# Kernel optimization log

Hardware: AMD Instinct MI355X
Metric: run time of the kernel (lower is better)

Reference implementation:

```python
import jax, jax.numpy as jnp
import numpy as np

B, N, DIN, DOUT, L = 32, 512, 768, 256, 512
NEG = -9.0e15
SLOPE = 0.2  # LeakyReLU negative slope


def setup_inputs() -> dict:
    key = jax.random.key(0)
    ks = jax.random.split(key, 7)
    h = jax.random.normal(ks[0], (B, N, DIN), dtype=jnp.float32)
    adj = jax.random.randint(ks[1], (B, N, N), 0, 2, dtype=jnp.int32)
    positions = jax.random.randint(ks[2], (B, N), 0, L, dtype=jnp.int32)
    W = jax.random.normal(ks[3], (DIN, DOUT), dtype=jnp.float32) * 0.02
    a1 = jax.random.normal(ks[4], (DOUT,), dtype=jnp.float32) * 0.02
    a2 = jax.random.normal(ks[5], (DOUT,), dtype=jnp.float32) * 0.02
    pos_table = jax.random.normal(ks[6], (L, DOUT), dtype=jnp.float32) * 0.02
    return {"h": h, "adj": adj, "positions": positions, "W": W,
            "a1": a1, "a2": a2, "pos_table": pos_table}


def reference(h, adj, positions, W, a1, a2, pos_table):
    # Wh = W(h) + pos_emb(positions)   -> [B, N, DOUT]
    Wh = jnp.einsum('bnd,de->bne', h, W) + pos_table[positions]
    # Pairwise GAT score: e_ij = leakyrelu(a1 . Wh_i + a2 . Wh_j)
    # (identical math to concat([Wh_i, Wh_j]) @ [a1; a2], without the O(N^2*2D) tensor)
    s1 = jnp.einsum('bnd,d->bn', Wh, a1)  # source term   [B, N]
    s2 = jnp.einsum('bnd,d->bn', Wh, a2)  # target term   [B, N]
    e = jax.nn.leaky_relu(s1[:, :, None] + s2[:, None, :], negative_slope=SLOPE)  # [B,N,N]
    # adjacency mask + softmax over neighbors (dropout is identity in eval)
    attention = jax.nn.softmax(jnp.where(adj > 0, e, NEG), axis=-1)  # [B, N, N]
    h_prime = jnp.einsum('bij,bjd->bid', attention, Wh)  # [B, N, DOUT]
    return h_prime, attention
```

## Files before the change

kernel.cpp:

```cpp
#include <hip/hip_runtime.h>
#include <math.h>

#define B 32
#define N 512
#define DIN 768
#define DOUT 256
#define NEGV -9.0e15f
#define SLOPE 0.2f

typedef __bf16 bf16x8 __attribute__((ext_vector_type(8)));
typedef float f32x4 __attribute__((ext_vector_type(4)));
typedef unsigned short us8 __attribute__((ext_vector_type(8)));

__device__ __forceinline__ unsigned short f2b(float f) {
    union { float f; unsigned u; } v; v.f = f;
    unsigned r = v.u + 0x7FFF + ((v.u >> 16) & 1);
    return (unsigned short)(r >> 16);
}

__device__ __forceinline__ void gload_lds16(const unsigned short* g, unsigned short* l) {
    __builtin_amdgcn_global_load_lds(
        (const __attribute__((address_space(1))) unsigned int*)(unsigned long long)(uintptr_t)g,
        (__attribute__((address_space(3))) unsigned int*)(uintptr_t)l,
        16, 0, 0);
}

__global__ __launch_bounds__(256) void conv_fused(
    const float4* __restrict__ hin, ushort4* __restrict__ hout,
    const float* __restrict__ W, unsigned short* __restrict__ WT) {
    __shared__ unsigned short tile[64][65];
    const int t = threadIdx.x;
    if (blockIdx.x < 12288) {
        int idx = blockIdx.x * 256 + t;
        float4 v = hin[idx];
        ushort4 o;
        o.x = f2b(v.x); o.y = f2b(v.y); o.z = f2b(v.z); o.w = f2b(v.w);
        hout[idx] = o;
    } else {
        int bid = blockIdx.x - 12288;
        int k0 = (bid % 12) * 64, n0 = (bid / 12) * 64;
        const int cl = t & 63, cg = t >> 6;
#pragma unroll
        for (int i = 0; i < 16; ++i) {
            int k = cg * 16 + i;
            tile[cl][k] = f2b(W[(size_t)(k0 + k) * DOUT + n0 + cl]);
        }
        __syncthreads();
#pragma unroll
        for (int i = 0; i < 16; ++i) {
            int n = cg * 16 + i;
            WT[(size_t)(n0 + n) * DIN + k0 + cl] = tile[n][cl];
        }
    }
}

__global__ __launch_bounds__(256) void wh_mfma(
    const unsigned short* __restrict__ hA,
    const unsigned short* __restrict__ WT,
    const int*   __restrict__ pos,
    const float* __restrict__ ptab,
    const float* __restrict__ a1,
    const float* __restrict__ a2,
    unsigned short* __restrict__ WhT,
    float* __restrict__ s1, float* __restrict__ s2)
{
    constexpr int K = DIN;
    __shared__ unsigned short smem[12288];
    unsigned short* As = smem;
    unsigned short* Bs = smem + 8192;
    unsigned short* tileT = smem;

    const int t    = threadIdx.x;
    const int lane = t & 63;
    const int w    = t >> 6;
    const int lin  = blockIdx.x;
    const int m0   = (lin & 127) * 128;
    const int n0   = (lin >> 7) * 64;

    int arow[4], apos[4];
#pragma unroll
    for (int i = 0; i < 4; ++i) {
        int c = i * 256 + t;
        arow[i] = c >> 3;
        apos[i] = (c & 7) ^ ((c >> 3) & 7);
    }
    int brow[2], bpos[2];
#pragma unroll
    for (int i = 0; i < 2; ++i) {
        int c = i * 256 + t;
        brow[i] = c >> 3;
        bpos[i] = (c & 7) ^ ((c >> 3) & 7);
    }
    const unsigned short* gA[4];
    const unsigned short* gB[2];
#pragma unroll
    for (int i = 0; i < 4; ++i) gA[i] = hA + (size_t)(m0 + arow[i]) * K + apos[i] * 8;
#pragma unroll
    for (int i = 0; i < 2; ++i) gB[i] = WT + (size_t)(n0 + brow[i]) * K + bpos[i] * 8;
    unsigned short* lA[4];
    unsigned short* lB[2];
#pragma unroll
    for (int i = 0; i < 4; ++i) lA[i] = As + (i * 256 + (t & 192)) * 8;
#pragma unroll
    for (int i = 0; i < 2; ++i) lB[i] = Bs + (i * 256 + (t & 192)) * 8;

    const int wm = (w & 1) * 64, wn = (w >> 1) * 32;
    const int l15 = lane & 15, q = lane >> 4;
    int aoff[2][4], boff[2][2];
#pragma unroll
    for (int kk = 0; kk < 2; ++kk) {
        int pg = kk * 4 + q;
#pragma unroll
        for (int i = 0; i < 4; ++i) {
            int rm = wm + i * 16 + l15;
            aoff[kk][i] = rm * 64 + ((pg ^ (rm & 7)) * 8);
        }
#pragma unroll
        for (int i = 0; i < 2; ++i) {
            int rn = wn + i * 16 + l15;
            boff[kk][i] = rn * 64 + ((pg ^ (rn & 7)) * 8);
        }
    }

    f32x4 acc[4][2];
#pragma unroll
    for (int i = 0; i < 4; ++i)
#pragma unroll
        for (int j = 0; j < 2; ++j) acc[i][j] = (f32x4){0.f, 0.f, 0.f, 0.f};

    for (int k0 = 0; k0 < K; k0 += 64) {
#pragma unroll
        for (int i = 0; i < 4; ++i) gload_lds16(gA[i] + k0, lA[i]);
#pragma unroll
        for (int i = 0; i < 2; ++i) gload_lds16(gB[i] + k0, lB[i]);
        __syncthreads();
#pragma unroll
        for (int kk = 0; kk < 2; ++kk) {
            bf16x8 af[4], bfr[2];
#pragma unroll
            for (int i = 0; i < 4; ++i) af[i] = *(const bf16x8*)(As + aoff[kk][i]);
#pragma unroll
            for (int i = 0; i < 2; ++i) bfr[i] = *(const bf16x8*)(Bs + boff[kk][i]);
#pragma unroll
            for (int mi = 0; mi < 4; ++mi)
#pragma unroll
                for (int ni = 0; ni < 2; ++ni)
                    acc[mi][ni] = __builtin_amdgcn_mfma_f32_16x16x32_bf16(
                        af[mi], bfr[ni], acc[mi][ni], 0, 0, 0);
        }
        __syncthreads();
    }

    const float a1v[2] = { a1[n0 + wn + l15], a1[n0 + wn + 16 + l15] };
    const float a2v[2] = { a2[n0 + wn + l15], a2[n0 + wn + 16 + l15] };
#pragma unroll
    for (int mi = 0; mi < 4; ++mi) {
        const int jb = wm + mi * 16 + q * 4;
        float v[2][4];
#pragma unroll
        for (int ni = 0; ni < 2; ++ni) {
            const int nl = wn + ni * 16 + l15;
            ushort4 pk;
            unsigned short* pp = (unsigned short*)&pk;
#pragma unroll
            for (int r = 0; r < 4; ++r) {
                int m = m0 + jb + r;
                int p = pos[m];
                float val = acc[mi][ni][r] + ptab[(size_t)p * DOUT + n0 + nl];
                v[ni][r] = val;
                pp[r] = f2b(val);
            }
            *(ushort4*)&tileT[nl * 136 + jb] = pk;
        }
#pragma unroll
        for (int r = 0; r < 4; ++r) {
            float t1 = v[0][r] * a1v[0] + v[1][r] * a1v[1];
            float t2 = v[0][r] * a2v[0] + v[1][r] * a2v[1];
#pragma unroll
            for (int mk = 1; mk < 16; mk <<= 1) {
                t1 += __shfl_xor(t1, mk);
                t2 += __shfl_xor(t2, mk);
            }
            if (l15 == 0) {
                atomicAdd(&s1[m0 + jb + r], t1);
                atomicAdd(&s2[m0 + jb + r], t2);
            }
        }
    }
    __syncthreads();
    const int bb = m0 >> 9, j0 = m0 & 511;
#pragma unroll
    for (int rr = 0; rr < 4; ++rr) {
        int nl = (t >> 4) + rr * 16;
        int jl = (t & 15) * 8;
        us8 vv = *(const us8*)&tileT[nl * 136 + jl];
        *(us8*)&WhT[((size_t)bb * DOUT + n0 + nl) * N + j0 + jl] = vv;
    }
}

__global__ __launch_bounds__(1024) void attn_hp(
    const float* __restrict__ s1,
    const float* __restrict__ s2,
    const int*   __restrict__ adj,
    const unsigned short* __restrict__ WhT,
    float* __restrict__ att,
    float* __restrict__ hp)
{
    __shared__ unsigned short P[64 * 512];

    const int t    = threadIdx.x;
    const int lane = t & 63;
    const int w    = t >> 6;
    const int xid  = blockIdx.x & 7;
    const int rid  = blockIdx.x >> 3;
    const int bb   = xid * 4 + (rid >> 3);
    const int m0   = (rid & 7) * 64;

    {
        const int r = t >> 4, c = t & 15;
        const size_t rowg = (size_t)bb * N + m0 + r;
        const float s1i = s1[rowg];
        const int4*   adjp = (const int4*)(adj + rowg * N) + c;
        const float4* s2p  = (const float4*)(s2 + (size_t)bb * N) + c;

        unsigned msk = 0u;
        float mx = -3.0e38f;
#pragma unroll
        for (int i = 0; i < 8; ++i) {
            int4 a = adjp[i * 16];
            float4 sv = s2p[i * 16];
            float v0 = s1i + sv.x; v0 = v0 > 0.f ? v0 : SLOPE * v0;
            float v1 = s1i + sv.y; v1 = v1 > 0.f ? v1 : SLOPE * v1;
            float v2 = s1i + sv.z; v2 = v2 > 0.f ? v2 : SLOPE * v2;
            float v3 = s1i + sv.w; v3 = v3 > 0.f ? v3 : SLOPE * v3;
            v0 = (a.x > 0) ? v0 : NEGV;
            v1 = (a.y > 0) ? v1 : NEGV;
            v2 = (a.z > 0) ? v2 : NEGV;
            v3 = (a.w > 0) ? v3 : NEGV;
            unsigned bits = (a.x > 0 ? 1u : 0u) | (a.y > 0 ? 2u : 0u) |
                            (a.z > 0 ? 4u : 0u) | (a.w > 0 ? 8u : 0u);
            msk |= bits << (i * 4);
            mx = fmaxf(mx, fmaxf(fmaxf(v0, v1), fmaxf(v2, v3)));
        }
#pragma unroll
        for (int mk = 1; mk < 16; mk <<= 1) mx = fmaxf(mx, __shfl_xor(mx, mk));

        float sum = 0.f;
#pragma unroll
        for (int i = 0; i < 8; ++i) {
            float4 sv = s2p[i * 16];
            float v0 = s1i + sv.x; v0 = v0 > 0.f ? v0 : SLOPE * v0;
            float v1 = s1i + sv.y; v1 = v1 > 0.f ? v1 : SLOPE * v1;
            float v2 = s1i + sv.z; v2 = v2 > 0.f ? v2 : SLOPE * v2;
            float v3 = s1i + sv.w; v3 = v3 > 0.f ? v3 : SLOPE * v3;
            v0 = ((msk >> (i * 4 + 0)) & 1) ? v0 : NEGV;
            v1 = ((msk >> (i * 4 + 1)) & 1) ? v1 : NEGV;
            v2 = ((msk >> (i * 4 + 2)) & 1) ? v2 : NEGV;
            v3 = ((msk >> (i * 4 + 3)) & 1) ? v3 : NEGV;
            sum += __expf(v0 - mx) + __expf(v1 - mx) +
                   __expf(v2 - mx) + __expf(v3 - mx);
        }
#pragma unroll
        for (int mk = 1; mk < 16; mk <<= 1) sum += __shfl_xor(sum, mk);
        const float inv = 1.0f / sum;

        float4* attrow = (float4*)(att + rowg * N);
        unsigned short* Prow = P + r * 512;
        const int r7 = r & 7, chalf = (c & 1) * 4;
#pragma unroll
        for (int i = 0; i < 8; ++i) {
            float4 sv = s2p[i * 16];
            float v0 = s1i + sv.x; v0 = v0 > 0.f ? v0 : SLOPE * v0;
            float v1 = s1i + sv.y; v1 = v1 > 0.f ? v1 : SLOPE * v1;
            float v2 = s1i + sv.z; v2 = v2 > 0.f ? v2 : SLOPE * v2;
            float v3 = s1i + sv.w; v3 = v3 > 0.f ? v3 : SLOPE * v3;
            v0 = ((msk >> (i * 4 + 0)) & 1) ? v0 : NEGV;
            v1 = ((msk >> (i * 4 + 1)) & 1) ? v1 : NEGV;
            v2 = ((msk >> (i * 4 + 2)) & 1) ? v2 : NEGV;
            v3 = ((msk >> (i * 4 + 3)) & 1) ? v3 : NEGV;
            float e0 = __expf(v0 - mx) * inv;
            float e1 = __expf(v1 - mx) * inv;
            float e2 = __expf(v2 - mx) * inv;
            float e3 = __expf(v3 - mx) * inv;
            attrow[i * 16 + c] = (float4){e0, e1, e2, e3};
            int slot = i * 8 + (c >> 1);
            int S = slot ^ r7 ^ (slot >> 3);
            ushort4 pk = { f2b(e0), f2b(e1), f2b(e2), f2b(e3) };
            *(ushort4*)&Prow[S * 8 + chalf] = pk;
        }
    }
    __syncthreads();

    const int wn  = w * 16;
    const int l15 = lane & 15, q = lane >> 4;
    const unsigned short* bRow = WhT + ((size_t)bb * DOUT + wn + l15) * N + q * 8;
    int rm7[4], rmBase[4];
#pragma unroll
    for (int mi = 0; mi < 4; ++mi) {
        int rm = mi * 16 + l15;
        rm7[mi] = rm & 7;
        rmBase[mi] = rm * 512;
    }

    f32x4 acc[4];
#pragma unroll
    for (int i = 0; i < 4; ++i) acc[i] = (f32x4){0.f, 0.f, 0.f, 0.f};

#pragma unroll 4
    for (int k0 = 0; k0 < N; k0 += 32) {
        const int slot = (k0 >> 3) + q;
        const int hi = slot >> 3;
        bf16x8 af[4];
        bf16x8 bfr = *(const bf16x8*)(bRow + k0);
#pragma unroll
        for (int mi = 0; mi < 4; ++mi) {
            int S = slot ^ rm7[mi] ^ hi;
            af[mi] = *(const bf16x8*)&P[rmBase[mi] + S * 8];
        }
#pragma unroll
        for (int mi = 0; mi < 4; ++mi)
            acc[mi] = __builtin_amdgcn_mfma_f32_16x16x32_bf16(
                af[mi], bfr, acc[mi], 0, 0, 0);
    }

#pragma unroll
    for (int mi = 0; mi < 4; ++mi) {
#pragma unroll
        for (int rr = 0; rr < 4; ++rr) {
            int m = m0 + mi * 16 + q * 4 + rr;
            int n = wn + l15;
            hp[((size_t)bb * N + m) * DOUT + n] = acc[mi][rr];
        }
    }
}

extern "C" void kernel_launch(void* const* d_in, const int* in_sizes, int n_in,
                              void* d_out, int out_size, void* d_ws, size_t ws_size,
                              hipStream_t stream) {
    const float* h         = (const float*)d_in[0];
    const int*   adj       = (const int*)  d_in[1];
    const int*   positions = (const int*)  d_in[2];
    const float* W         = (const float*)d_in[3];
    const float* a1        = (const float*)d_in[4];
    const float* a2        = (const float*)d_in[5];
    const float* pos_table = (const float*)d_in[6];

    float* out     = (float*)d_out;
    float* h_prime = out;
    float* att     = out + (size_t)B * N * DOUT;

    char* ws = (char*)d_ws;
    unsigned short* h_bf = (unsigned short*)ws;
    unsigned short* WT   = (unsigned short*)(ws + 25165824);
    unsigned short* WhT  = (unsigned short*)(ws + 25559040);
    float*          s1   = (float*)(ws + 33947648);
    float*          s2   = s1 + (size_t)B * N;

    hipMemsetAsync(s1, 0, (size_t)2 * B * N * sizeof(float), stream);
    conv_fused<<<12288 + 48, 256, 0, stream>>>((const float4*)h, (ushort4*)h_bf, W, WT);
    wh_mfma<<<512, 256, 0, stream>>>(h_bf, WT, positions, pos_table, a1, a2, WhT, s1, s2);
    attn_hp<<<256, 1024, 0, stream>>>(s1, s2, adj, WhT, att, h_prime);
}
```

Measured before the change: 164.1 us.

## Fuse fp32-to-bf16 conversion of h into the Wh GEMM A-tile load

Removes the separate pass that converted h to bf16 in a workspace buffer. The GEMM now reads fp32 h directly with register loads, converts to bf16 in registers, and writes the swizzled tile to LDS. This avoids writing and re-reading a 25 MB intermediate. The cost is that the A loads go through registers instead of the async global-to-LDS path, and they read twice the bytes per tile.

```diff
diff --git a/kernel.cpp b/kernel.cpp
--- a/kernel.cpp
+++ b/kernel.cpp
@@ -25,37 +25,28 @@
         16, 0, 0);
 }
 
-__global__ __launch_bounds__(256) void conv_fused(
-    const float4* __restrict__ hin, ushort4* __restrict__ hout,
+__global__ __launch_bounds__(256) void wt_kernel(
     const float* __restrict__ W, unsigned short* __restrict__ WT) {
     __shared__ unsigned short tile[64][65];
     const int t = threadIdx.x;
-    if (blockIdx.x < 12288) {
-        int idx = blockIdx.x * 256 + t;
-        float4 v = hin[idx];
-        ushort4 o;
-        o.x = f2b(v.x); o.y = f2b(v.y); o.z = f2b(v.z); o.w = f2b(v.w);
-        hout[idx] = o;
-    } else {
-        int bid = blockIdx.x - 12288;
-        int k0 = (bid % 12) * 64, n0 = (bid / 12) * 64;
-        const int cl = t & 63, cg = t >> 6;
-#pragma unroll
-        for (int i = 0; i < 16; ++i) {
-            int k = cg * 16 + i;
-            tile[cl][k] = f2b(W[(size_t)(k0 + k) * DOUT + n0 + cl]);
-        }
-        __syncthreads();
-#pragma unroll
-        for (int i = 0; i < 16; ++i) {
-            int n = cg * 16 + i;
-            WT[(size_t)(n0 + n) * DIN + k0 + cl] = tile[n][cl];
-        }
+    int bid = blockIdx.x;
+    int k0 = (bid % 12) * 64, n0 = (bid / 12) * 64;
+    const int cl = t & 63, cg = t >> 6;
+#pragma unroll
+    for (int i = 0; i < 16; ++i) {
+        int k = cg * 16 + i;
+        tile[cl][k] = f2b(W[(size_t)(k0 + k) * DOUT + n0 + cl]);
+    }
+    __syncthreads();
+#pragma unroll
+    for (int i = 0; i < 16; ++i) {
+        int n = cg * 16 + i;
+        WT[(size_t)(n0 + n) * DIN + k0 + cl] = tile[n][cl];
     }
 }
 
 __global__ __launch_bounds__(256) void wh_mfma(
-    const unsigned short* __restrict__ hA,
+    const float* __restrict__ hF,
     const unsigned short* __restrict__ WT,
     const int*   __restrict__ pos,
     const float* __restrict__ ptab,
@@ -77,32 +68,26 @@
     const int m0   = (lin & 127) * 128;
     const int n0   = (lin >> 7) * 64;
 
-    int arow[4], apos[4];
+    const float* gA[4];
+    int aw[4];
 #pragma unroll
     for (int i = 0; i < 4; ++i) {
         int c = i * 256 + t;
-        arow[i] = c >> 3;
-        apos[i] = (c & 7) ^ ((c >> 3) & 7);
-    }
-    int brow[2], bpos[2];
+        int arow = c >> 3;
+        int apos = (c & 7) ^ (arow & 7);
+        gA[i] = hF + (size_t)(m0 + arow) * K + apos * 8;
+        aw[i] = c * 8;
+    }
+    const unsigned short* gB[2];
+    unsigned short* lB[2];
 #pragma unroll
     for (int i = 0; i < 2; ++i) {
         int c = i * 256 + t;
-        brow[i] = c >> 3;
-        bpos[i] = (c & 7) ^ ((c >> 3) & 7);
-    }
-    const unsigned short* gA[4];
-    const unsigned short* gB[2];
-#pragma unroll
-    for (int i = 0; i < 4; ++i) gA[i] = hA + (size_t)(m0 + arow[i]) * K + apos[i] * 8;
-#pragma unroll
-    for (int i = 0; i < 2; ++i) gB[i] = WT + (size_t)(n0 + brow[i]) * K + bpos[i] * 8;
-    unsigned short* lA[4];
-    unsigned short* lB[2];
-#pragma unroll
-    for (int i = 0; i < 4; ++i) lA[i] = As + (i * 256 + (t & 192)) * 8;
-#pragma unroll
-    for (int i = 0; i < 2; ++i) lB[i] = Bs + (i * 256 + (t & 192)) * 8;
+        int brow = c >> 3;
+        int bpos = (c & 7) ^ (brow & 7);
+        gB[i] = WT + (size_t)(n0 + brow) * K + bpos * 8;
+        lB[i] = Bs + (i * 256 + (t & 192)) * 8;
+    }
 
     const int wm = (w & 1) * 64, wn = (w >> 1) * 32;
     const int l15 = lane & 15, q = lane >> 4;
@@ -129,10 +114,23 @@
         for (int j = 0; j < 2; ++j) acc[i][j] = (f32x4){0.f, 0.f, 0.f, 0.f};
 
     for (int k0 = 0; k0 < K; k0 += 64) {
-#pragma unroll
-        for (int i = 0; i < 4; ++i) gload_lds16(gA[i] + k0, lA[i]);
+        float4 f0[4], f1[4];
+#pragma unroll
+        for (int i = 0; i < 4; ++i) {
+            f0[i] = *(const float4*)(gA[i] + k0);
+            f1[i] = *(const float4*)(gA[i] + k0 + 4);
+        }
 #pragma unroll
         for (int i = 0; i < 2; ++i) gload_lds16(gB[i] + k0, lB[i]);
+#pragma unroll
+        for (int i = 0; i < 4; ++i) {
+            union { us8 v; __bf16 b[8]; } p;
+            p.b[0] = (__bf16)f0[i].x; p.b[1] = (__bf16)f0[i].y;
+            p.b[2] = (__bf16)f0[i].z; p.b[3] = (__bf16)f0[i].w;
+            p.b[4] = (__bf16)f1[i].x; p.b[5] = (__bf16)f1[i].y;
+            p.b[6] = (__bf16)f1[i].z; p.b[7] = (__bf16)f1[i].w;
+            *(us8*)(As + aw[i]) = p.v;
+        }
         __syncthreads();
 #pragma unroll
         for (int kk = 0; kk < 2; ++kk) {
@@ -350,14 +348,13 @@
     float* att     = out + (size_t)B * N * DOUT;
 
     char* ws = (char*)d_ws;
-    unsigned short* h_bf = (unsigned short*)ws;
-    unsigned short* WT   = (unsigned short*)(ws + 25165824);
-    unsigned short* WhT  = (unsigned short*)(ws + 25559040);
-    float*          s1   = (float*)(ws + 33947648);
-    float*          s2   = s1 + (size_t)B * N;
+    unsigned short* WT  = (unsigned short*)ws;
+    unsigned short* WhT = (unsigned short*)(ws + 393216);
+    float*          s1  = (float*)(ws + 8781824);
+    float*          s2  = s1 + (size_t)B * N;
 
     hipMemsetAsync(s1, 0, (size_t)2 * B * N * sizeof(float), stream);
-    conv_fused<<<12288 + 48, 256, 0, stream>>>((const float4*)h, (ushort4*)h_bf, W, WT);
-    wh_mfma<<<512, 256, 0, stream>>>(h_bf, WT, positions, pos_table, a1, a2, WhT, s1, s2);
+    wt_kernel<<<48, 256, 0, stream>>>(W, WT);
+    wh_mfma<<<512, 256, 0, stream>>>(h, WT, positions, pos_table, a1, a2, WhT, s1, s2);
     attn_hp<<<256, 1024, 0, stream>>>(s1, s2, adj, WhT, att, h_prime);
 }
```

Measured after the change: 164.3 us. About the same (+0.1%).
